# Optimization experiments

Hardware: AMD Instinct MI355X
Metric: run time of the kernel (lower is better)

## Reference

```python
import jax, jax.numpy as jnp
import numpy as np

B, S, D, H = 2, 4096, 512, 8
DH = D // H
EPS = 1e-5


def setup_inputs() -> dict:
    key = jax.random.key(0)
    ks = jax.random.split(key, 8)
    s = 0.02
    return {
        "x": jax.random.normal(ks[0], (B, S, D), jnp.float32),
        "in_proj_w": jax.random.normal(ks[1], (3 * D, D), jnp.float32) * s,
        "in_proj_b": jnp.zeros((3 * D,), jnp.float32),
        "out_proj_w": jax.random.normal(ks[2], (D, D), jnp.float32) * s,
        "out_proj_b": jnp.zeros((D,), jnp.float32),
        "ln1_g": jnp.ones((D,), jnp.float32),
        "ln1_b": jnp.zeros((D,), jnp.float32),
        "ln2_g": jnp.ones((D,), jnp.float32),
        "ln2_b": jnp.zeros((D,), jnp.float32),
        "w1": jax.random.normal(ks[3], (D, D), jnp.float32) * s,
        "b1": jnp.zeros((D,), jnp.float32),
        "w2": jax.random.normal(ks[4], (D, D), jnp.float32) * s,
        "b2": jnp.zeros((D,), jnp.float32),
        "window": 256,
    }


def _layernorm(x, g, b):
    mu = jnp.mean(x, axis=-1, keepdims=True)
    var = jnp.mean(jnp.square(x - mu), axis=-1, keepdims=True)
    return (x - mu) * jax.lax.rsqrt(var + EPS) * g + b


def reference(x, in_proj_w, in_proj_b, out_proj_w, out_proj_b,
              ln1_g, ln1_b, ln2_g, ln2_b, w1, b1, w2, b2, window):
    b, s, d = x.shape
    # sliding-window mask: allowed iff |i - j| <= window
    idx = jnp.arange(s)
    allowed = jnp.abs(idx[:, None] - idx[None, :]) <= window  # [S,S]

    # fused QKV projection (torch MultiheadAttention layout: W [3D, D])
    qkv = x @ in_proj_w.T + in_proj_b  # [B,S,3D]
    q, k, v = jnp.split(qkv, 3, axis=-1)
    q = q.reshape(b, s, H, DH)
    k = k.reshape(b, s, H, DH)
    v = v.reshape(b, s, H, DH)

    scale = 1.0 / jnp.sqrt(jnp.float32(DH))
    scores = jnp.einsum("bqhd,bkhd->bhqk", q, k) * scale  # [B,H,S,S]
    scores = jnp.where(allowed[None, None], scores, -jnp.inf)
    attn = jax.nn.softmax(scores, axis=-1)
    ctx = jnp.einsum("bhqk,bkhd->bqhd", attn, v).reshape(b, s, d)
    attn_out = ctx @ out_proj_w.T + out_proj_b

    # residual + LayerNorm (dropout rate 0 -> identity)
    h = _layernorm(x + attn_out, ln1_g, ln1_b)
    mlp = jax.nn.relu(h @ w1.T + b1) @ w2.T + b2
    return _layernorm(h + mlp, ln2_g, ln2_b)
```

## Files before the change

kernel.cpp:

```cpp
#include <hip/hip_runtime.h>

typedef __bf16 bf16;
typedef __bf16 bf16x2 __attribute__((ext_vector_type(2)));
typedef __bf16 bf16x8 __attribute__((ext_vector_type(8)));
typedef float f32x4 __attribute__((ext_vector_type(4)));

#define S_LEN 4096
#define DMODEL 512
#define NHEAD 8
#define DHEAD 64
#define BATCH 2
#define M_ROWS (BATCH * S_LEN)
#define K_DIM 512
#define QLD 512

__device__ __forceinline__ void async16(void* lds, const void* g) {
  __builtin_amdgcn_global_load_lds(
      (const __attribute__((address_space(1))) unsigned int*)g,
      (__attribute__((address_space(3))) unsigned int*)lds, 16, 0, 0);
}

__device__ __forceinline__ int detect_bf16(const unsigned int* x, int lane) {
  int cnt = 0;
#pragma unroll
  for (int i = 0; i < 16; ++i) {
    const unsigned int w = x[lane * 16 + i];
    const unsigned int e = (w >> 7) & 0xFFu;
    cnt += (e >= 100u && e <= 140u) ? 1 : 0;
  }
#pragma unroll
  for (int off = 1; off < 64; off <<= 1) cnt += __shfl_xor(cnt, off);
  return (cnt >= 700) ? 1 : 0;
}

__device__ __forceinline__ bf16x8 ld8(const void* p, size_t e, bool asF32) {
  if (asF32) {
    const float* q = (const float*)p + e;
    const float4 a = *(const float4*)q;
    const float4 b = *(const float4*)(q + 4);
    bf16x8 r;
    r[0] = (bf16)a.x; r[1] = (bf16)a.y; r[2] = (bf16)a.z; r[3] = (bf16)a.w;
    r[4] = (bf16)b.x; r[5] = (bf16)b.y; r[6] = (bf16)b.z; r[7] = (bf16)b.w;
    return r;
  }
  return *(const bf16x8*)((const bf16*)p + e);
}

__device__ __forceinline__ float ld1(const void* p, size_t e, bool asF32) {
  return asF32 ? ((const float*)p)[e] : (float)((const bf16*)p)[e];
}

__global__ __launch_bounds__(256) void cvt_all(const void* __restrict__ x,
                                               const void* __restrict__ s0,
                                               const void* __restrict__ s1,
                                               const void* __restrict__ s2,
                                               const void* __restrict__ s3,
                                               bf16* __restrict__ xb,
                                               bf16* __restrict__ warena,
                                               int* __restrict__ flag) {
  const int isbf = detect_bf16((const unsigned int*)x, threadIdx.x & 63);
  const bool f32in = (isbf == 0);
  const int b = blockIdx.x;
  if (b == 0 && threadIdx.x == 0) *flag = isbf;
  if (b < 2048) {
    const size_t idx = ((size_t)b * 256 + threadIdx.x) * 8;
    *(bf16x8*)(xb + idx) = ld8(x, idx, f32in);
    return;
  }
  const int wb = b - 2048;
  const void* s;
  size_t doff;
  int lb;
  if (wb < 384)      { s = s0; doff = 0;        lb = wb; }
  else if (wb < 512) { s = s1; doff = 786432;   lb = wb - 384; }
  else if (wb < 640) { s = s2; doff = 1048576;  lb = wb - 512; }
  else               { s = s3; doff = 1310720;  lb = wb - 640; }
  const size_t idx = (size_t)lb * 2048 + threadIdx.x * 8;
  *(bf16x8*)(warena + doff + idx) = ld8(s, idx, f32in);
}

__global__ __launch_bounds__(256) void gemm_qkv(const bf16* __restrict__ A,
                                                const bf16* __restrict__ W,
                                                const void* __restrict__ bias,
                                                bf16* __restrict__ C,
                                                const int* __restrict__ flag) {
  __shared__ __align__(16) bf16 As[128 * 64];
  __shared__ __align__(16) bf16 Ws[128 * 64];

  const bool f32in = (*flag == 0);
  const int t = threadIdx.x;
  const int lane = t & 63;
  const int wave = t >> 6;
  const int wm = (wave >> 1) * 64;
  const int wn = (wave & 1) * 64;
  const int l16 = lane & 15;
  const int quad = lane >> 4;

  constexpr int NB = 1536 / 128;
  const int bid = blockIdx.x;
  const int xcd = bid & 7;
  const int r = bid >> 3;
  const int m0 = (xcd * 8 + r / NB) * 128;
  const int n0 = (r % NB) * 128;

  const int rr = lane >> 3;
  const int cb = (lane & 7) ^ rr;
  const int sw = l16 & 7;

  f32x4 acc[4][4];
#pragma unroll
  for (int i = 0; i < 4; ++i)
#pragma unroll
    for (int j = 0; j < 4; ++j) acc[i][j] = (f32x4){0.f, 0.f, 0.f, 0.f};

  for (int kt = 0; kt < K_DIM; kt += 64) {
    __syncthreads();
#pragma unroll
    for (int i = 0; i < 4; ++i) {
      const int r0 = wave * 32 + i * 8;
      async16(&As[r0 * 64], &A[(size_t)(m0 + r0 + rr) * K_DIM + kt + cb * 8]);
    }
#pragma unroll
    for (int i = 0; i < 4; ++i) {
      const int r0 = wave * 32 + i * 8;
      async16(&Ws[r0 * 64], &W[(size_t)(n0 + r0 + rr) * K_DIM + kt + cb * 8]);
    }
    __syncthreads();
#pragma unroll
    for (int ks = 0; ks < 2; ++ks) {
      bf16x8 af[4], wf[4];
#pragma unroll
      for (int mt = 0; mt < 4; ++mt)
        af[mt] = *(const bf16x8*)&As[(wm + mt * 16 + l16) * 64 +
                                     (((ks * 4 + quad) ^ sw) * 8)];
#pragma unroll
      for (int nt = 0; nt < 4; ++nt)
        wf[nt] = *(const bf16x8*)&Ws[(wn + nt * 16 + l16) * 64 +
                                     (((ks * 4 + quad) ^ sw) * 8)];
#pragma unroll
      for (int mt = 0; mt < 4; ++mt)
#pragma unroll
        for (int nt = 0; nt < 4; ++nt)
          acc[mt][nt] = __builtin_amdgcn_mfma_f32_16x16x32_bf16(af[mt], wf[nt],
                                                                acc[mt][nt], 0, 0, 0);
    }
  }

#pragma unroll
  for (int nt = 0; nt < 4; ++nt) {
    const int n = n0 + wn + nt * 16 + l16;
    const float bv = ld1(bias, n, f32in);
    bf16* Cm = C + (size_t)(n >> 9) * ((size_t)M_ROWS * DMODEL) + (n & 511);
#pragma unroll
    for (int mt = 0; mt < 4; ++mt) {
#pragma unroll
      for (int r4 = 0; r4 < 4; ++r4) {
        const int m = m0 + wm + mt * 16 + quad * 4 + r4;
        Cm[(size_t)m * DMODEL] = (bf16)(acc[mt][nt][r4] + bv);
      }
    }
  }
}

__global__ __launch_bounds__(256) void attn_fwd(bf16* __restrict__ qkv,
                                                const int* __restrict__ wptr) {
  __shared__ __align__(16) bf16 Kt[2][64 * 64];
  __shared__ __align__(16) bf16 Vt[2][64][72];
  __shared__ __align__(16) bf16 Pbuf[4][16][72];

  const bf16* Q = qkv;
  const bf16* K = qkv + (size_t)M_ROWS * DMODEL;
  const bf16* V = qkv + 2 * (size_t)M_ROWS * DMODEL;
  bf16* ctxw = qkv;

  const int t = threadIdx.x;
  const int lane = t & 63;
  const int wave = t >> 6;
  const int l16 = lane & 15;
  const int quad = lane >> 4;
  const int rr = lane >> 3;
  const int cb = (lane & 7) ^ rr;
  const int sw = l16 & 7;

  const int bid = blockIdx.x;
  const int xcd = bid & 7;
  const int jj = bid >> 3;
  const int pair = xcd * 2 + (jj >> 6);
  const int qblk = jj & 63;
  const int h = pair & 7;
  const int b = pair >> 3;
  const int qbase = qblk * 64;
  int window = *wptr;
  if (window < 0) window = 0;
  if (window > S_LEN) window = S_LEN;
  const float sc_log2e = 0.125f * 1.44269504f;

  const int qrow = qbase + wave * 16 + l16;
  const bf16* qp = Q + (size_t)(b * S_LEN + qrow) * QLD + h * DHEAD;
  const bf16x8 qf0 = *(const bf16x8*)(qp + quad * 8);
  const bf16x8 qf1 = *(const bf16x8*)(qp + 32 + quad * 8);

  f32x4 o[4];
#pragma unroll
  for (int nt = 0; nt < 4; ++nt) o[nt] = (f32x4){0.f, 0.f, 0.f, 0.f};
  float lp[4] = {0.f, 0.f, 0.f, 0.f};

  int kstart = qbase - window;
  if (kstart < 0) kstart = 0;
  kstart &= ~63;
  int kend = qbase + 64 + window;
  if (kend > S_LEN) kend = S_LEN;
  const int niter = (kend - kstart + 63) >> 6;

  const int vk = (t & 31) * 2;
  const int vd = (t >> 5) * 8;
  const bf16* vbase = V + (size_t)(b * S_LEN) * QLD + h * DHEAD + vd;
  const bf16* kbase = K + (size_t)(b * S_LEN) * QLD + h * DHEAD;

#pragma unroll
  for (int i = 0; i < 2; ++i) {
    const int r0 = wave * 16 + i * 8;
    async16(&Kt[0][r0 * 64],
            &kbase[(size_t)(kstart + r0 + rr) * QLD + cb * 8]);
  }
  {
    const bf16* p = vbase + (size_t)(kstart + vk) * QLD;
    const bf16x8 va = *(const bf16x8*)p;
    const bf16x8 vb = *(const bf16x8*)(p + QLD);
#pragma unroll
    for (int j = 0; j < 8; ++j) {
      bf16x2 pr; pr[0] = va[j]; pr[1] = vb[j];
      *(bf16x2*)&Vt[0][vd + j][vk] = pr;
    }
  }

  for (int it = 0; it < niter; ++it) {
    const int kt = kstart + it * 64;
    const int cur = it & 1;
    __syncthreads();

    bf16x8 na, nb;
    const bool have_next = (it + 1 < niter);
    if (have_next) {
#pragma unroll
      for (int i = 0; i < 2; ++i) {
        const int r0 = wave * 16 + i * 8;
        async16(&Kt[cur ^ 1][r0 * 64],
                &kbase[(size_t)(kt + 64 + r0 + rr) * QLD + cb * 8]);
      }
      const bf16* p = vbase + (size_t)(kt + 64 + vk) * QLD;
      na = *(const bf16x8*)p;
      nb = *(const bf16x8*)(p + QLD);
    }

    f32x4 s[4];
#pragma unroll
    for (int t4 = 0; t4 < 4; ++t4) s[t4] = (f32x4){0.f, 0.f, 0.f, 0.f};

    __builtin_amdgcn_s_setprio(1);
#pragma unroll
    for (int t4 = 0; t4 < 4; ++t4) {
      const int row = t4 * 16 + l16;
      const bf16x8 k0 = *(const bf16x8*)&Kt[cur][row * 64 + ((quad ^ sw) * 8)];
      const bf16x8 k1 =
          *(const bf16x8*)&Kt[cur][row * 64 + (((4 + quad) ^ sw) * 8)];
      s[t4] = __builtin_amdgcn_mfma_f32_16x16x32_bf16(qf0, k0, s[t4], 0, 0, 0);
      s[t4] = __builtin_amdgcn_mfma_f32_16x16x32_bf16(qf1, k1, s[t4], 0, 0, 0);
    }
    __builtin_amdgcn_s_setprio(0);

#pragma unroll
    for (int r = 0; r < 4; ++r) {
      const int q = qbase + wave * 16 + quad * 4 + r;
      const int lo = q - window, hi = q + window;
#pragma unroll
      for (int t4 = 0; t4 < 4; ++t4) {
        const int key = kt + t4 * 16 + l16;
        const float p = (key >= lo && key <= hi)
                            ? __builtin_amdgcn_exp2f(s[t4][r] * sc_log2e)
                            : 0.f;
        lp[r] += p;
        Pbuf[wave][quad * 4 + r][t4 * 16 + l16] = (bf16)p;
      }
    }

    const bf16x8 pf0 = *(const bf16x8*)&Pbuf[wave][l16][quad * 8];
    const bf16x8 pf1 = *(const bf16x8*)&Pbuf[wave][l16][32 + quad * 8];
    __builtin_amdgcn_s_setprio(1);
#pragma unroll
    for (int nt = 0; nt < 4; ++nt) {
      const bf16x8 v0 = *(const bf16x8*)&Vt[cur][nt * 16 + l16][quad * 8];
      const bf16x8 v1 = *(const bf16x8*)&Vt[cur][nt * 16 + l16][32 + quad * 8];
      o[nt] = __builtin_amdgcn_mfma_f32_16x16x32_bf16(pf0, v0, o[nt], 0, 0, 0);
      o[nt] = __builtin_amdgcn_mfma_f32_16x16x32_bf16(pf1, v1, o[nt], 0, 0, 0);
    }
    __builtin_amdgcn_s_setprio(0);

    if (have_next) {
#pragma unroll
      for (int j = 0; j < 8; ++j) {
        bf16x2 pr; pr[0] = na[j]; pr[1] = nb[j];
        *(bf16x2*)&Vt[cur ^ 1][vd + j][vk] = pr;
      }
    }
  }

#pragma unroll
  for (int r = 0; r < 4; ++r) {
#pragma unroll
    for (int off = 1; off < 16; off <<= 1) lp[r] += __shfl_xor(lp[r], off);
    const float inv = (lp[r] > 0.f) ? (1.0f / lp[r]) : 0.f;
    const int q = qbase + wave * 16 + quad * 4 + r;
#pragma unroll
    for (int nt = 0; nt < 4; ++nt) {
      ctxw[(size_t)(b * S_LEN + q) * QLD + h * DHEAD + nt * 16 + l16] =
          (bf16)(o[nt][r] * inv);
    }
  }
}

__global__ __launch_bounds__(512, 1) void fused_tail(
    const bf16* __restrict__ ctxg, const void* __restrict__ x,
    const bf16* __restrict__ wo, const bf16* __restrict__ w1m,
    const bf16* __restrict__ w2m, const void* __restrict__ bo,
    const void* __restrict__ g1, const void* __restrict__ be1,
    const void* __restrict__ b1p, const void* __restrict__ b2p,
    const void* __restrict__ g2, const void* __restrict__ be2,
    void* __restrict__ out, const int* __restrict__ flag) {
  __shared__ __align__(16) bf16 AL0[32 * 512];
  __shared__ __align__(16) bf16 hL[32 * 512];
  __shared__ __align__(16) bf16 Wslab[2][512 * 32];
  float* red = (float*)AL0;

  const bool f32in = (*flag == 0);
  const int t = threadIdx.x;
  const int lane = t & 63;
  const int wave = t >> 6;
  const int l16 = lane & 15;
  const int quad = lane >> 4;
  const int wcol = wave * 64;
  const int rowbase = blockIdx.x * 32;

#pragma unroll
  for (int j = 0; j < 4; ++j) {
    const int dgi = j * 512 + t;
    const int row = dgi >> 6, g = dgi & 63;
    async16(&AL0[dgi * 8],
            &ctxg[(size_t)(rowbase + row) * 512 + ((g ^ (row & 7)) * 8)]);
  }
  auto stageW = [&](int buf, int s) {
    const bf16* wsrc = (s < 16) ? wo : (s < 32) ? w1m : w2m;
    const int kt = (s & 15) * 32;
#pragma unroll
    for (int j = 0; j < 4; ++j) {
      const int dgi = j * 512 + t;
      const int n = dgi >> 2, g = dgi & 3;
      async16(&Wslab[buf][dgi * 8],
              &wsrc[(size_t)n * 512 + kt + ((g ^ ((n >> 1) & 3)) * 8)]);
    }
  };
  stageW(0, 0);

  f32x4 acc[2][4];
  auto zeroAcc = [&]() {
#pragma unroll
    for (int mt = 0; mt < 2; ++mt)
#pragma unroll
      for (int ct = 0; ct < 4; ++ct) acc[mt][ct] = (f32x4){0.f, 0.f, 0.f, 0.f};
  };
  zeroAcc();

  auto computeStep = [&](const bf16* AL, int s) {
    const int gb = (s & 15) * 4;
    bf16x8 af[2], wfv[4];
#pragma unroll
    for (int mt = 0; mt < 2; ++mt) {
      const int row = mt * 16 + l16;
      af[mt] = *(const bf16x8*)&AL[row * 512 + (((gb + quad) ^ (row & 7)) * 8)];
    }
    const bf16* WB = &Wslab[s & 1][0];
#pragma unroll
    for (int ct = 0; ct < 4; ++ct) {
      const int n = wcol + ct * 16 + l16;
      wfv[ct] = *(const bf16x8*)&WB[n * 32 + ((quad ^ ((n >> 1) & 3)) * 8)];
    }
#pragma unroll
    for (int mt = 0; mt < 2; ++mt)
#pragma unroll
      for (int ct = 0; ct < 4; ++ct)
        acc[mt][ct] = __builtin_amdgcn_mfma_f32_16x16x32_bf16(
            af[mt], wfv[ct], acc[mt][ct], 0, 0, 0);
  };

  int s = 0;
  for (int i = 0; i < 16; ++i, ++s) {
    __syncthreads();
    stageW((s + 1) & 1, s + 1);
    computeStep(AL0, s);
  }

  float hreg[2][4][4];
  {
    float vv[2][4][4], ps[2][4], ps2[2][4];
#pragma unroll
    for (int mt = 0; mt < 2; ++mt)
#pragma unroll
      for (int r = 0; r < 4; ++r) { ps[mt][r] = 0.f; ps2[mt][r] = 0.f; }
#pragma unroll
    for (int mt = 0; mt < 2; ++mt)
#pragma unroll
      for (int ct = 0; ct < 4; ++ct) {
        const int col = wcol + ct * 16 + l16;
        const float bov = ld1(bo, col, f32in);
#pragma unroll
        for (int r = 0; r < 4; ++r) {
          const int row = mt * 16 + quad * 4 + r;
          const float xv = ld1(x, (size_t)(rowbase + row) * 512 + col, f32in);
          const float v = acc[mt][ct][r] + bov + xv;
          vv[mt][ct][r] = v;
          ps[mt][r] += v;
          ps2[mt][r] += v * v;
        }
      }
#pragma unroll
    for (int mt = 0; mt < 2; ++mt)
#pragma unroll
      for (int r = 0; r < 4; ++r)
#pragma unroll
        for (int off = 1; off < 16; off <<= 1) {
          ps[mt][r] += __shfl_xor(ps[mt][r], off);
          ps2[mt][r] += __shfl_xor(ps2[mt][r], off);
        }
    __syncthreads();
    if (l16 == 0) {
#pragma unroll
      for (int mt = 0; mt < 2; ++mt)
#pragma unroll
        for (int r = 0; r < 4; ++r) {
          const int row = mt * 16 + quad * 4 + r;
          red[(row * 8 + wave) * 2 + 0] = ps[mt][r];
          red[(row * 8 + wave) * 2 + 1] = ps2[mt][r];
        }
    }
    __syncthreads();
    float mean[2][4], rstd[2][4];
#pragma unroll
    for (int mt = 0; mt < 2; ++mt)
#pragma unroll
      for (int r = 0; r < 4; ++r) {
        const int row = mt * 16 + quad * 4 + r;
        float sm = 0.f, sq = 0.f;
#pragma unroll
        for (int w = 0; w < 8; ++w) {
          sm += red[(row * 8 + w) * 2 + 0];
          sq += red[(row * 8 + w) * 2 + 1];
        }
        const float mu = sm * (1.f / 512.f);
        float var = sq * (1.f / 512.f) - mu * mu;
        if (var < 0.f) var = 0.f;
        mean[mt][r] = mu;
        rstd[mt][r] = rsqrtf(var + 1e-5f);
      }
#pragma unroll
    for (int mt = 0; mt < 2; ++mt)
#pragma unroll
      for (int ct = 0; ct < 4; ++ct) {
        const int col = wcol + ct * 16 + l16;
        const float gv = ld1(g1, col, f32in);
        const float bv = ld1(be1, col, f32in);
#pragma unroll
        for (int r = 0; r < 4; ++r) {
          const int row = mt * 16 + quad * 4 + r;
          const float hv = (vv[mt][ct][r] - mean[mt][r]) * rstd[mt][r] * gv + bv;
          hreg[mt][ct][r] = hv;
          hL[row * 512 + (((col >> 3) ^ (row & 7)) * 8) + (col & 7)] = (bf16)hv;
        }
      }
  }
  zeroAcc();

  for (int i = 0; i < 16; ++i, ++s) {
    __syncthreads();
    stageW((s + 1) & 1, s + 1);
    computeStep(hL, s);
  }
  {
#pragma unroll
    for (int mt = 0; mt < 2; ++mt)
#pragma unroll
      for (int ct = 0; ct < 4; ++ct) {
        const int col = wcol + ct * 16 + l16;
        const float b1v = ld1(b1p, col, f32in);
#pragma unroll
        for (int r = 0; r < 4; ++r) {
          const int row = mt * 16 + quad * 4 + r;
          const float a = fmaxf(acc[mt][ct][r] + b1v, 0.f);
          AL0[row * 512 + (((col >> 3) ^ (row & 7)) * 8) + (col & 7)] = (bf16)a;
        }
      }
  }
  zeroAcc();

  for (int i = 0; i < 16; ++i, ++s) {
    __syncthreads();
    if (s + 1 < 48) stageW((s + 1) & 1, s + 1);
    computeStep(AL0, s);
  }
  __syncthreads();

  {
    float vv[2][4][4], ps[2][4], ps2[2][4];
#pragma unroll
    for (int mt = 0; mt < 2; ++mt)
#pragma unroll
      for (int r = 0; r < 4; ++r) { ps[mt][r] = 0.f; ps2[mt][r] = 0.f; }
#pragma unroll
    for (int mt = 0; mt < 2; ++mt)
#pragma unroll
      for (int ct = 0; ct < 4; ++ct) {
        const int col = wcol + ct * 16 + l16;
        const float b2v = ld1(b2p, col, f32in);
#pragma unroll
        for (int r = 0; r < 4; ++r) {
          const float v = acc[mt][ct][r] + b2v + hreg[mt][ct][r];
          vv[mt][ct][r] = v;
          ps[mt][r] += v;
          ps2[mt][r] += v * v;
        }
      }
#pragma unroll
    for (int mt = 0; mt < 2; ++mt)
#pragma unroll
      for (int r = 0; r < 4; ++r)
#pragma unroll
        for (int off = 1; off < 16; off <<= 1) {
          ps[mt][r] += __shfl_xor(ps[mt][r], off);
          ps2[mt][r] += __shfl_xor(ps2[mt][r], off);
        }
    if (l16 == 0) {
#pragma unroll
      for (int mt = 0; mt < 2; ++mt)
#pragma unroll
        for (int r = 0; r < 4; ++r) {
          const int row = mt * 16 + quad * 4 + r;
          red[(row * 8 + wave) * 2 + 0] = ps[mt][r];
          red[(row * 8 + wave) * 2 + 1] = ps2[mt][r];
        }
    }
    __syncthreads();
#pragma unroll
    for (int mt = 0; mt < 2; ++mt)
#pragma unroll
      for (int r = 0; r < 4; ++r) {
        const int row = mt * 16 + quad * 4 + r;
        float sm = 0.f, sq = 0.f;
#pragma unroll
        for (int w = 0; w < 8; ++w) {
          sm += red[(row * 8 + w) * 2 + 0];
          sq += red[(row * 8 + w) * 2 + 1];
        }
        const float mu = sm * (1.f / 512.f);
        float var = sq * (1.f / 512.f) - mu * mu;
        if (var < 0.f) var = 0.f;
        const float rs = rsqrtf(var + 1e-5f);
#pragma unroll
        for (int ct = 0; ct < 4; ++ct) {
          const int col = wcol + ct * 16 + l16;
          const float gv = ld1(g2, col, f32in);
          const float bv = ld1(be2, col, f32in);
          const float ov = (vv[mt][ct][r] - mu) * rs * gv + bv;
          if (f32in)
            ((float*)out)[(size_t)(rowbase + row) * 512 + col] = ov;
          else
            ((bf16*)out)[(size_t)(rowbase + row) * 512 + col] = (bf16)ov;
        }
      }
  }
}

extern "C" void kernel_launch(void* const* d_in, const int* in_sizes, int n_in,
                              void* d_out, int out_size, void* d_ws, size_t ws_size,
                              hipStream_t stream) {
  const void* x          = d_in[0];
  const void* in_proj_w  = d_in[1];
  const void* in_proj_b  = d_in[2];
  const void* out_proj_w = d_in[3];
  const void* out_proj_b = d_in[4];
  const void* ln1_g      = d_in[5];
  const void* ln1_b      = d_in[6];
  const void* ln2_g      = d_in[7];
  const void* ln2_b      = d_in[8];
  const void* w1         = d_in[9];
  const void* b1         = d_in[10];
  const void* w2         = d_in[11];
  const void* b2         = d_in[12];
  const int*  wptr       = (const int*)d_in[13];

  char* ws = (char*)d_ws;
  int* flag = (int*)ws;
  bf16* warena = (bf16*)(ws + 256);
  bf16* wq  = warena;
  bf16* wo  = warena + 786432;
  bf16* w1b = warena + 1048576;
  bf16* w2b = warena + 1310720;
  bf16* qkvS = (bf16*)(ws + 256 + 3145728);
  bf16* xb   = (bf16*)d_out;

  cvt_all<<<2816, 256, 0, stream>>>(x, in_proj_w, out_proj_w, w1, w2, xb, warena, flag);
  gemm_qkv<<<768, 256, 0, stream>>>(xb, wq, in_proj_b, qkvS, flag);
  attn_fwd<<<dim3(BATCH * NHEAD * (S_LEN / 64)), 256, 0, stream>>>(qkvS, wptr);
  fused_tail<<<256, 512, 0, stream>>>(qkvS, x, wo, w1b, w2b, out_proj_b,
                                      ln1_g, ln1_b, b1, b2, ln2_g, ln2_b,
                                      d_out, flag);
}
```

Measured before the change: 208.7 us.

## Retile fused tail to 16-row blocks of 4 waves with single LDS activation buffer

The fused out-proj/LN/MLP/LN tail kernel now processes 16 rows per block with 256 threads (4 waves, each covering 128 output columns) instead of 32 rows with 512 threads, and launches 512 blocks. The separate hL buffer is removed and the single AL0 buffer is reused for h and the ReLU activation, with extra barriers added to make that reuse safe. Each block fits in less LDS, so two blocks can be resident per CU and more blocks are available to fill the GPU. In exchange each weight slab staged into LDS is used by half as many rows, which doubles total weight traffic, and there are extra barriers.

Measured after the change: 216.6 us. +3.8%, slower.

```diff
diff --git a/kernel.cpp b/kernel.cpp
--- a/kernel.cpp
+++ b/kernel.cpp
@@ -319,7 +319,7 @@
   }
 }
 
-__global__ __launch_bounds__(512, 1) void fused_tail(
+__global__ __launch_bounds__(256, 2) void fused_tail(
     const bf16* __restrict__ ctxg, const void* __restrict__ x,
     const bf16* __restrict__ wo, const bf16* __restrict__ w1m,
     const bf16* __restrict__ w2m, const void* __restrict__ bo,
@@ -327,8 +327,7 @@
     const void* __restrict__ b1p, const void* __restrict__ b2p,
     const void* __restrict__ g2, const void* __restrict__ be2,
     void* __restrict__ out, const int* __restrict__ flag) {
-  __shared__ __align__(16) bf16 AL0[32 * 512];
-  __shared__ __align__(16) bf16 hL[32 * 512];
+  __shared__ __align__(16) bf16 AL0[16 * 512];
   __shared__ __align__(16) bf16 Wslab[2][512 * 32];
   float* red = (float*)AL0;
 
@@ -338,12 +337,12 @@
   const int wave = t >> 6;
   const int l16 = lane & 15;
   const int quad = lane >> 4;
-  const int wcol = wave * 64;
-  const int rowbase = blockIdx.x * 32;
+  const int wcol = wave * 128;
+  const int rowbase = blockIdx.x * 16;
 
 #pragma unroll
   for (int j = 0; j < 4; ++j) {
-    const int dgi = j * 512 + t;
+    const int dgi = j * 256 + t;
     const int row = dgi >> 6, g = dgi & 63;
     async16(&AL0[dgi * 8],
             &ctxg[(size_t)(rowbase + row) * 512 + ((g ^ (row & 7)) * 8)]);
@@ -352,8 +351,8 @@
     const bf16* wsrc = (s < 16) ? wo : (s < 32) ? w1m : w2m;
     const int kt = (s & 15) * 32;
 #pragma unroll
-    for (int j = 0; j < 4; ++j) {
-      const int dgi = j * 512 + t;
+    for (int j = 0; j < 8; ++j) {
+      const int dgi = j * 256 + t;
       const int n = dgi >> 2, g = dgi & 3;
       async16(&Wslab[buf][dgi * 8],
               &wsrc[(size_t)n * 512 + kt + ((g ^ ((n >> 1) & 3)) * 8)]);
@@ -361,220 +360,184 @@
   };
   stageW(0, 0);
 
-  f32x4 acc[2][4];
+  f32x4 acc[8];
   auto zeroAcc = [&]() {
 #pragma unroll
-    for (int mt = 0; mt < 2; ++mt)
-#pragma unroll
-      for (int ct = 0; ct < 4; ++ct) acc[mt][ct] = (f32x4){0.f, 0.f, 0.f, 0.f};
+    for (int ct = 0; ct < 8; ++ct) acc[ct] = (f32x4){0.f, 0.f, 0.f, 0.f};
   };
   zeroAcc();
 
-  auto computeStep = [&](const bf16* AL, int s) {
+  auto computeStep = [&](int s) {
     const int gb = (s & 15) * 4;
-    bf16x8 af[2], wfv[4];
-#pragma unroll
-    for (int mt = 0; mt < 2; ++mt) {
-      const int row = mt * 16 + l16;
-      af[mt] = *(const bf16x8*)&AL[row * 512 + (((gb + quad) ^ (row & 7)) * 8)];
-    }
+    const bf16x8 af =
+        *(const bf16x8*)&AL0[l16 * 512 + (((gb + quad) ^ (l16 & 7)) * 8)];
     const bf16* WB = &Wslab[s & 1][0];
 #pragma unroll
-    for (int ct = 0; ct < 4; ++ct) {
+    for (int ct = 0; ct < 8; ++ct) {
       const int n = wcol + ct * 16 + l16;
-      wfv[ct] = *(const bf16x8*)&WB[n * 32 + ((quad ^ ((n >> 1) & 3)) * 8)];
-    }
-#pragma unroll
-    for (int mt = 0; mt < 2; ++mt)
-#pragma unroll
-      for (int ct = 0; ct < 4; ++ct)
-        acc[mt][ct] = __builtin_amdgcn_mfma_f32_16x16x32_bf16(
-            af[mt], wfv[ct], acc[mt][ct], 0, 0, 0);
+      const bf16x8 wf =
+          *(const bf16x8*)&WB[n * 32 + ((quad ^ ((n >> 1) & 3)) * 8)];
+      acc[ct] = __builtin_amdgcn_mfma_f32_16x16x32_bf16(af, wf, acc[ct], 0, 0, 0);
+    }
   };
 
   int s = 0;
   for (int i = 0; i < 16; ++i, ++s) {
     __syncthreads();
     stageW((s + 1) & 1, s + 1);
-    computeStep(AL0, s);
-  }
-
-  float hreg[2][4][4];
+    computeStep(s);
+  }
+
+  float hreg[8][4];
   {
-    float vv[2][4][4], ps[2][4], ps2[2][4];
-#pragma unroll
-    for (int mt = 0; mt < 2; ++mt)
-#pragma unroll
-      for (int r = 0; r < 4; ++r) { ps[mt][r] = 0.f; ps2[mt][r] = 0.f; }
-#pragma unroll
-    for (int mt = 0; mt < 2; ++mt)
-#pragma unroll
-      for (int ct = 0; ct < 4; ++ct) {
+    float vv[8][4], ps[4] = {0, 0, 0, 0}, ps2[4] = {0, 0, 0, 0};
+#pragma unroll
+    for (int ct = 0; ct < 8; ++ct) {
+      const int col = wcol + ct * 16 + l16;
+      const float bov = ld1(bo, col, f32in);
+#pragma unroll
+      for (int r = 0; r < 4; ++r) {
+        const int row = quad * 4 + r;
+        const float xv = ld1(x, (size_t)(rowbase + row) * 512 + col, f32in);
+        const float v = acc[ct][r] + bov + xv;
+        vv[ct][r] = v;
+        ps[r] += v;
+        ps2[r] += v * v;
+      }
+    }
+#pragma unroll
+    for (int r = 0; r < 4; ++r)
+#pragma unroll
+      for (int off = 1; off < 16; off <<= 1) {
+        ps[r] += __shfl_xor(ps[r], off);
+        ps2[r] += __shfl_xor(ps2[r], off);
+      }
+    __syncthreads();
+    if (l16 == 0) {
+#pragma unroll
+      for (int r = 0; r < 4; ++r) {
+        const int row = quad * 4 + r;
+        red[(row * 4 + wave) * 2 + 0] = ps[r];
+        red[(row * 4 + wave) * 2 + 1] = ps2[r];
+      }
+    }
+    __syncthreads();
+    float mean[4], rstd[4];
+#pragma unroll
+    for (int r = 0; r < 4; ++r) {
+      const int row = quad * 4 + r;
+      float sm = 0.f, sq = 0.f;
+#pragma unroll
+      for (int w = 0; w < 4; ++w) {
+        sm += red[(row * 4 + w) * 2 + 0];
+        sq += red[(row * 4 + w) * 2 + 1];
+      }
+      const float mu = sm * (1.f / 512.f);
+      float var = sq * (1.f / 512.f) - mu * mu;
+      if (var < 0.f) var = 0.f;
+      mean[r] = mu;
+      rstd[r] = rsqrtf(var + 1e-5f);
+    }
+    __syncthreads();
+#pragma unroll
+    for (int ct = 0; ct < 8; ++ct) {
+      const int col = wcol + ct * 16 + l16;
+      const float gv = ld1(g1, col, f32in);
+      const float bv = ld1(be1, col, f32in);
+#pragma unroll
+      for (int r = 0; r < 4; ++r) {
+        const int row = quad * 4 + r;
+        const float hv = (vv[ct][r] - mean[r]) * rstd[r] * gv + bv;
+        hreg[ct][r] = hv;
+        AL0[row * 512 + (((col >> 3) ^ (row & 7)) * 8) + (col & 7)] = (bf16)hv;
+      }
+    }
+  }
+  zeroAcc();
+
+  for (int i = 0; i < 16; ++i, ++s) {
+    __syncthreads();
+    stageW((s + 1) & 1, s + 1);
+    computeStep(s);
+  }
+  __syncthreads();
+  {
+#pragma unroll
+    for (int ct = 0; ct < 8; ++ct) {
+      const int col = wcol + ct * 16 + l16;
+      const float b1v = ld1(b1p, col, f32in);
+#pragma unroll
+      for (int r = 0; r < 4; ++r) {
+        const int row = quad * 4 + r;
+        const float a = fmaxf(acc[ct][r] + b1v, 0.f);
+        AL0[row * 512 + (((col >> 3) ^ (row & 7)) * 8) + (col & 7)] = (bf16)a;
+      }
+    }
+  }
+  zeroAcc();
+
+  for (int i = 0; i < 16; ++i, ++s) {
+    __syncthreads();
+    if (s + 1 < 48) stageW((s + 1) & 1, s + 1);
+    computeStep(s);
+  }
+  __syncthreads();
+
+  {
+    float vv[8][4], ps[4] = {0, 0, 0, 0}, ps2[4] = {0, 0, 0, 0};
+#pragma unroll
+    for (int ct = 0; ct < 8; ++ct) {
+      const int col = wcol + ct * 16 + l16;
+      const float b2v = ld1(b2p, col, f32in);
+#pragma unroll
+      for (int r = 0; r < 4; ++r) {
+        const float v = acc[ct][r] + b2v + hreg[ct][r];
+        vv[ct][r] = v;
+        ps[r] += v;
+        ps2[r] += v * v;
+      }
+    }
+#pragma unroll
+    for (int r = 0; r < 4; ++r)
+#pragma unroll
+      for (int off = 1; off < 16; off <<= 1) {
+        ps[r] += __shfl_xor(ps[r], off);
+        ps2[r] += __shfl_xor(ps2[r], off);
+      }
+    if (l16 == 0) {
+#pragma unroll
+      for (int r = 0; r < 4; ++r) {
+        const int row = quad * 4 + r;
+        red[(row * 4 + wave) * 2 + 0] = ps[r];
+        red[(row * 4 + wave) * 2 + 1] = ps2[r];
+      }
+    }
+    __syncthreads();
+#pragma unroll
+    for (int r = 0; r < 4; ++r) {
+      const int row = quad * 4 + r;
+      float sm = 0.f, sq = 0.f;
+#pragma unroll
+      for (int w = 0; w < 4; ++w) {
+        sm += red[(row * 4 + w) * 2 + 0];
+        sq += red[(row * 4 + w) * 2 + 1];
+      }
+      const float mu = sm * (1.f / 512.f);
+      float var = sq * (1.f / 512.f) - mu * mu;
+      if (var < 0.f) var = 0.f;
+      const float rs = rsqrtf(var + 1e-5f);
+#pragma unroll
+      for (int ct = 0; ct < 8; ++ct) {
         const int col = wcol + ct * 16 + l16;
-        const float bov = ld1(bo, col, f32in);
-#pragma unroll
-        for (int r = 0; r < 4; ++r) {
-          const int row = mt * 16 + quad * 4 + r;
-          const float xv = ld1(x, (size_t)(rowbase + row) * 512 + col, f32in);
-          const float v = acc[mt][ct][r] + bov + xv;
-          vv[mt][ct][r] = v;
-          ps[mt][r] += v;
-          ps2[mt][r] += v * v;
-        }
-      }
-#pragma unroll
-    for (int mt = 0; mt < 2; ++mt)
-#pragma unroll
-      for (int r = 0; r < 4; ++r)
-#pragma unroll
-        for (int off = 1; off < 16; off <<= 1) {
-          ps[mt][r] += __shfl_xor(ps[mt][r], off);
-          ps2[mt][r] += __shfl_xor(ps2[mt][r], off);
-        }
-    __syncthreads();
-    if (l16 == 0) {
-#pragma unroll
-      for (int mt = 0; mt < 2; ++mt)
-#pragma unroll
-        for (int r = 0; r < 4; ++r) {
-          const int row = mt * 16 + quad * 4 + r;
-          red[(row * 8 + wave) * 2 + 0] = ps[mt][r];
-          red[(row * 8 + wave) * 2 + 1] = ps2[mt][r];
-        }
-    }
-    __syncthreads();
-    float mean[2][4], rstd[2][4];
-#pragma unroll
-    for (int mt = 0; mt < 2; ++mt)
-#pragma unroll
-      for (int r = 0; r < 4; ++r) {
-        const int row = mt * 16 + quad * 4 + r;
-        float sm = 0.f, sq = 0.f;
-#pragma unroll
-        for (int w = 0; w < 8; ++w) {
-          sm += red[(row * 8 + w) * 2 + 0];
-          sq += red[(row * 8 + w) * 2 + 1];
-        }
-        const float mu = sm * (1.f / 512.f);
-        float var = sq * (1.f / 512.f) - mu * mu;
-        if (var < 0.f) var = 0.f;
-        mean[mt][r] = mu;
-        rstd[mt][r] = rsqrtf(var + 1e-5f);
-      }
-#pragma unroll
-    for (int mt = 0; mt < 2; ++mt)
-#pragma unroll
-      for (int ct = 0; ct < 4; ++ct) {
-        const int col = wcol + ct * 16 + l16;
-        const float gv = ld1(g1, col, f32in);
-        const float bv = ld1(be1, col, f32in);
-#pragma unroll
-        for (int r = 0; r < 4; ++r) {
-          const int row = mt * 16 + quad * 4 + r;
-          const float hv = (vv[mt][ct][r] - mean[mt][r]) * rstd[mt][r] * gv + bv;
-          hreg[mt][ct][r] = hv;
-          hL[row * 512 + (((col >> 3) ^ (row & 7)) * 8) + (col & 7)] = (bf16)hv;
-        }
-      }
-  }
-  zeroAcc();
-
-  for (int i = 0; i < 16; ++i, ++s) {
-    __syncthreads();
-    stageW((s + 1) & 1, s + 1);
-    computeStep(hL, s);
-  }
-  {
-#pragma unroll
-    for (int mt = 0; mt < 2; ++mt)
-#pragma unroll
-      for (int ct = 0; ct < 4; ++ct) {
-        const int col = wcol + ct * 16 + l16;
-        const float b1v = ld1(b1p, col, f32in);
-#pragma unroll
-        for (int r = 0; r < 4; ++r) {
-          const int row = mt * 16 + quad * 4 + r;
-          const float a = fmaxf(acc[mt][ct][r] + b1v, 0.f);
-          AL0[row * 512 + (((col >> 3) ^ (row & 7)) * 8) + (col & 7)] = (bf16)a;
-        }
-      }
-  }
-  zeroAcc();
-
-  for (int i = 0; i < 16; ++i, ++s) {
-    __syncthreads();
-    if (s + 1 < 48) stageW((s + 1) & 1, s + 1);
-    computeStep(AL0, s);
-  }
-  __syncthreads();
-
-  {
-    float vv[2][4][4], ps[2][4], ps2[2][4];
-#pragma unroll
-    for (int mt = 0; mt < 2; ++mt)
-#pragma unroll
-      for (int r = 0; r < 4; ++r) { ps[mt][r] = 0.f; ps2[mt][r] = 0.f; }
-#pragma unroll
-    for (int mt = 0; mt < 2; ++mt)
-#pragma unroll
-      for (int ct = 0; ct < 4; ++ct) {
-        const int col = wcol + ct * 16 + l16;
-        const float b2v = ld1(b2p, col, f32in);
-#pragma unroll
-        for (int r = 0; r < 4; ++r) {
-          const float v = acc[mt][ct][r] + b2v + hreg[mt][ct][r];
-          vv[mt][ct][r] = v;
-          ps[mt][r] += v;
-          ps2[mt][r] += v * v;
-        }
-      }
-#pragma unroll
-    for (int mt = 0; mt < 2; ++mt)
-#pragma unroll
-      for (int r = 0; r < 4; ++r)
-#pragma unroll
-        for (int off = 1; off < 16; off <<= 1) {
-          ps[mt][r] += __shfl_xor(ps[mt][r], off);
-          ps2[mt][r] += __shfl_xor(ps2[mt][r], off);
-        }
-    if (l16 == 0) {
-#pragma unroll
-      for (int mt = 0; mt < 2; ++mt)
-#pragma unroll
-        for (int r = 0; r < 4; ++r) {
-          const int row = mt * 16 + quad * 4 + r;
-          red[(row * 8 + wave) * 2 + 0] = ps[mt][r];
-          red[(row * 8 + wave) * 2 + 1] = ps2[mt][r];
-        }
-    }
-    __syncthreads();
-#pragma unroll
-    for (int mt = 0; mt < 2; ++mt)
-#pragma unroll
-      for (int r = 0; r < 4; ++r) {
-        const int row = mt * 16 + quad * 4 + r;
-        float sm = 0.f, sq = 0.f;
-#pragma unroll
-        for (int w = 0; w < 8; ++w) {
-          sm += red[(row * 8 + w) * 2 + 0];
-          sq += red[(row * 8 + w) * 2 + 1];
-        }
-        const float mu = sm * (1.f / 512.f);
-        float var = sq * (1.f / 512.f) - mu * mu;
-        if (var < 0.f) var = 0.f;
-        const float rs = rsqrtf(var + 1e-5f);
-#pragma unroll
-        for (int ct = 0; ct < 4; ++ct) {
-          const int col = wcol + ct * 16 + l16;
-          const float gv = ld1(g2, col, f32in);
-          const float bv = ld1(be2, col, f32in);
-          const float ov = (vv[mt][ct][r] - mu) * rs * gv + bv;
-          if (f32in)
-            ((float*)out)[(size_t)(rowbase + row) * 512 + col] = ov;
-          else
-            ((bf16*)out)[(size_t)(rowbase + row) * 512 + col] = (bf16)ov;
-        }
-      }
+        const float gv = ld1(g2, col, f32in);
+        const float bv = ld1(be2, col, f32in);
+        const float ov = (vv[ct][r] - mu) * rs * gv + bv;
+        if (f32in)
+          ((float*)out)[(size_t)(rowbase + row) * 512 + col] = ov;
+        else
+          ((bf16*)out)[(size_t)(rowbase + row) * 512 + col] = (bf16)ov;
+      }
+    }
   }
 }
 
@@ -609,7 +572,7 @@
   cvt_all<<<2816, 256, 0, stream>>>(x, in_proj_w, out_proj_w, w1, w2, xb, warena, flag);
   gemm_qkv<<<768, 256, 0, stream>>>(xb, wq, in_proj_b, qkvS, flag);
   attn_fwd<<<dim3(BATCH * NHEAD * (S_LEN / 64)), 256, 0, stream>>>(qkvS, wptr);
-  fused_tail<<<256, 512, 0, stream>>>(qkvS, x, wo, w1b, w2b, out_proj_b,
+  fused_tail<<<512, 256, 0, stream>>>(qkvS, x, wo, w1b, w2b, out_proj_b,
                                       ln1_g, ln1_b, b1, b2, ln2_g, ln2_b,
                                       d_out, flag);
 }
```
